# Kernel optimization log

Measured on AMD Instinct MI355X. Metric: run time of the kernel, lower is better.

The kernel has to match this reference:

```python
import jax, jax.numpy as jnp
import numpy as np

B, T = 16, 32768
N_FILTERS, FILTER_LEN = 30, 7


def _stable_coeffs(rng, n_filters, k):
    """Stable IIR denominators (a[0]=1, poles inside unit circle) + random numerators."""
    order = k - 1
    as_list = []
    for _ in range(n_filters):
        radii = rng.uniform(0.5, 0.95, order // 2)
        angles = rng.uniform(0.05, np.pi - 0.05, order // 2)
        poles = radii * np.exp(1j * angles)
        poles = np.concatenate([poles, poles.conj()])
        as_list.append(np.poly(poles).real)  # length k, a[0]=1
    as_ = np.stack(as_list).astype(np.float32)
    bs = (rng.normal(size=(n_filters, k)) * 0.1).astype(np.float32)
    return bs, as_


def setup_inputs() -> dict:
    key = jax.random.key(0)
    x = jax.random.normal(key, (B, T), dtype=jnp.float32)
    rng = np.random.default_rng(0)
    bs, as_ = _stable_coeffs(rng, N_FILTERS, FILTER_LEN)
    return {"x": x, "bs": jnp.asarray(bs), "as_": jnp.asarray(as_)}


def reference(x, bs, as_):
    # x: [B, T]; bs, as_: [F, K]. Output: [B, F, T]
    F, K = bs.shape
    Bb, Tt = x.shape
    a0 = as_[:, :1]
    b = bs / a0
    a_rest = (as_ / a0)[:, 1:]  # [F, K-1]

    # FIR part: fir[b,f,t] = sum_k b[f,k] * x[b, t-k]  (causal convolution)
    lhs = x[:, None, :]                      # [B, 1, T]
    kern = jnp.flip(b, axis=1)[:, None, :]   # [F, 1, K] (flip: conv, not corr)
    fir = jax.lax.conv_general_dilated(
        lhs, kern, window_strides=(1,), padding=[(K - 1, 0)],
        dimension_numbers=("NCH", "OIH", "NCH"))  # [B, F, T]

    # Recursive part: y[t] = fir[t] - sum_{k=1..K-1} a[k] * y[t-k]
    def step(ybuf, fir_t):
        # ybuf: [B, F, K-1] holds y[t-1], ..., y[t-(K-1)]
        y_t = fir_t - jnp.einsum("bfk,fk->bf", ybuf, a_rest)
        ybuf = jnp.concatenate([y_t[:, :, None], ybuf[:, :, :-1]], axis=2)
        return ybuf, y_t

    init = jnp.zeros((Bb, F, K - 1), dtype=x.dtype)
    _, ys = jax.lax.scan(step, init, jnp.moveaxis(fir, 2, 0))  # ys: [T, B, F]
    return jnp.transpose(ys, (1, 2, 0))  # [B, F, T]
```

## Files before the change

kernel.cpp:

```cpp
#include <hip/hip_runtime.h>


#define BB 16
#define TT 32768
#define FF 30
#define KK 7
#define ORD 6
#define CHUNK 64
#define WARM 128
#define CPB 2
#define TSPAN (CPB * CHUNK)
#define NBC (TT / TSPAN)
#define YSTR 132
#define XTILE (WARM + TSPAN)
#define BLK 64

__device__ __forceinline__ float iir_step(float xv, float st[ORD],
                                          const float bcf[KK],
                                          const float acf[ORD]) {
    float y = fmaf(bcf[0], xv, st[0]);
#pragma unroll
    for (int j = 0; j < ORD - 1; ++j)
        st[j] = fmaf(-acf[j], y, fmaf(bcf[j + 1], xv, st[j + 1]));
    st[ORD - 1] = fmaf(-acf[ORD - 1], y, bcf[KK - 1] * xv);
    return y;
}

__global__ __launch_bounds__(BLK) void iir_lds_kernel(
    const float* __restrict__ x,
    const float* __restrict__ bs,
    const float* __restrict__ as_,
    float* __restrict__ out)
{
    __shared__ __align__(16) float ly[FF * YSTR];
    __shared__ __align__(16) float lx[XTILE];

    const int tid = threadIdx.x;
    const int b   = blockIdx.x / NBC;
    const int bc  = blockIdx.x % NBC;
    const int bt0 = bc * TSPAN;
    const int xs  = bt0 - WARM;

    const float* __restrict__ xrow = x + b * TT;

    const int f  = tid % FF;
    const int cl = tid / FF;
    const bool active = tid < FF * CPB;

    float bcf[KK], acf[ORD];
    {
        const int fc = active ? f : 0;
        const float inv_a0 = 1.0f / as_[fc * KK];
#pragma unroll
        for (int j = 0; j < KK; ++j) bcf[j] = bs[fc * KK + j] * inv_a0;
#pragma unroll
        for (int j = 0; j < ORD; ++j) acf[j] = as_[fc * KK + 1 + j] * inv_a0;
    }

    {
        const int t = xs + 4 * tid;
        float4 v = make_float4(0.f, 0.f, 0.f, 0.f);
        if (t >= 0) v = *reinterpret_cast<const float4*>(xrow + t);
        *reinterpret_cast<float4*>(lx + 4 * tid) = v;
    }
    __syncthreads();

    if (active) {
        float st[ORD];
#pragma unroll
        for (int j = 0; j < ORD; ++j) st[j] = 0.0f;

        const float* lxc = lx + cl * CHUNK;

#pragma unroll 8
        for (int s = 0; s < WARM; s += 4) {
            const float4 v = *reinterpret_cast<const float4*>(lxc + s);
            iir_step(v.x, st, bcf, acf);
            iir_step(v.y, st, bcf, acf);
            iir_step(v.z, st, bcf, acf);
            iir_step(v.w, st, bcf, acf);
        }

        float* lyc = ly + f * YSTR + cl * CHUNK;
#pragma unroll 4
        for (int s = 0; s < CHUNK; s += 4) {
            const float4 v = *reinterpret_cast<const float4*>(lxc + WARM + s);
            float4 y;
            y.x = iir_step(v.x, st, bcf, acf);
            y.y = iir_step(v.y, st, bcf, acf);
            y.z = iir_step(v.z, st, bcf, acf);
            y.w = iir_step(v.w, st, bcf, acf);
            *reinterpret_cast<float4*>(lyc + s) = y;
        }
    }
    __syncthreads();

    float* __restrict__ obase = out + b * FF * TT + bt0;
#pragma unroll
    for (int it = 0; it < (FF * TSPAN / 4) / BLK; ++it) {
        const int j  = tid + BLK * it;
        const int fr = j >> 5;
        const int tl = (j & 31) << 2;
        const float4 v = *reinterpret_cast<const float4*>(ly + fr * YSTR + tl);
        *reinterpret_cast<float4*>(obase + fr * TT + tl) = v;
    }
}

extern "C" void kernel_launch(void* const* d_in, const int* in_sizes, int n_in,
                              void* d_out, int out_size, void* d_ws,
                              size_t ws_size, hipStream_t stream) {
    const float* x   = (const float*)d_in[0];
    const float* bs  = (const float*)d_in[1];
    const float* as_ = (const float*)d_in[2];
    float* out = (float*)d_out;

    const int grid = BB * NBC;
    hipLaunchKernelGGL(iir_lds_kernel, dim3(grid), dim3(BLK), 0, stream,
                       x, bs, as_, out);
}
```

Baseline: 29.35 us.

## Interleave two independent IIR chunks per thread and store outputs directly

Each block now covers 256 time steps, and each active thread runs two independent 64-sample chunks (each with a 128-sample warm-up) whose recurrence steps are interleaved to give instruction-level parallelism. The grid is halved. The LDS output staging buffer and the second barrier are removed, so threads write float4 results straight to global memory. In exchange, per-thread global stores are strided across filter rows and coalesce less well, and register pressure rises from the two state vectors.

```diff
diff --git a/kernel.cpp b/kernel.cpp
--- a/kernel.cpp
+++ b/kernel.cpp
@@ -6,13 +6,9 @@
 #define FF 30
 #define KK 7
 #define ORD 6
-#define CHUNK 64
-#define WARM 128
-#define CPB 2
-#define TSPAN (CPB * CHUNK)
+#define TSPAN 256
 #define NBC (TT / TSPAN)
-#define YSTR 132
-#define XTILE (WARM + TSPAN)
+#define XTILE (TSPAN + 128)
 #define BLK 64
 
 __device__ __forceinline__ float iir_step(float xv, float st[ORD],
@@ -26,26 +22,22 @@
     return y;
 }
 
-__global__ __launch_bounds__(BLK) void iir_lds_kernel(
+__global__ __launch_bounds__(BLK, 2) void iir_ilp2_kernel(
     const float* __restrict__ x,
     const float* __restrict__ bs,
     const float* __restrict__ as_,
     float* __restrict__ out)
 {
-    __shared__ __align__(16) float ly[FF * YSTR];
     __shared__ __align__(16) float lx[XTILE];
 
     const int tid = threadIdx.x;
     const int b   = blockIdx.x / NBC;
     const int bc  = blockIdx.x % NBC;
     const int bt0 = bc * TSPAN;
-    const int xs  = bt0 - WARM;
-
-    const float* __restrict__ xrow = x + b * TT;
 
     const int f  = tid % FF;
     const int cl = tid / FF;
-    const bool active = tid < FF * CPB;
+    const bool active = tid < FF * 2;
 
     float bcf[KK], acf[ORD];
     {
@@ -58,51 +50,51 @@
     }
 
     {
-        const int t = xs + 4 * tid;
-        float4 v = make_float4(0.f, 0.f, 0.f, 0.f);
-        if (t >= 0) v = *reinterpret_cast<const float4*>(xrow + t);
-        *reinterpret_cast<float4*>(lx + 4 * tid) = v;
+        const float* __restrict__ xrow = x + b * TT;
+#pragma unroll
+        for (int i = 0; i < 2; ++i) {
+            const int p = i * BLK + tid;
+            if (p < XTILE / 4) {
+                const int t = bt0 - 128 + 4 * p;
+                float4 v = make_float4(0.f, 0.f, 0.f, 0.f);
+                if (t >= 0) v = *reinterpret_cast<const float4*>(xrow + t);
+                *reinterpret_cast<float4*>(lx + 4 * p) = v;
+            }
+        }
     }
     __syncthreads();
 
     if (active) {
-        float st[ORD];
+        const float4* lx4 = reinterpret_cast<const float4*>(lx);
+        const int cA = cl;
+        const int cB = cl + 2;
+
+        float stA[ORD], stB[ORD];
 #pragma unroll
-        for (int j = 0; j < ORD; ++j) st[j] = 0.0f;
+        for (int j = 0; j < ORD; ++j) { stA[j] = 0.0f; stB[j] = 0.0f; }
 
-        const float* lxc = lx + cl * CHUNK;
+        float* __restrict__ orow = out + (b * FF + f) * TT + bt0;
+        float* __restrict__ oA = orow + 64 * cA;
+        float* __restrict__ oB = orow + 64 * cB;
 
-#pragma unroll 8
-        for (int s = 0; s < WARM; s += 4) {
-            const float4 v = *reinterpret_cast<const float4*>(lxc + s);
-            iir_step(v.x, st, bcf, acf);
-            iir_step(v.y, st, bcf, acf);
-            iir_step(v.z, st, bcf, acf);
-            iir_step(v.w, st, bcf, acf);
+#pragma unroll
+        for (int k = 0; k < 48; ++k) {
+            const float4 vA = lx4[16 * cA + k];
+            const float4 vB = lx4[16 * cB + k];
+            float4 yA, yB;
+            yA.x = iir_step(vA.x, stA, bcf, acf);
+            yB.x = iir_step(vB.x, stB, bcf, acf);
+            yA.y = iir_step(vA.y, stA, bcf, acf);
+            yB.y = iir_step(vB.y, stB, bcf, acf);
+            yA.z = iir_step(vA.z, stA, bcf, acf);
+            yB.z = iir_step(vB.z, stB, bcf, acf);
+            yA.w = iir_step(vA.w, stA, bcf, acf);
+            yB.w = iir_step(vB.w, stB, bcf, acf);
+            if (k >= 32) {
+                *reinterpret_cast<float4*>(oA + 4 * (k - 32)) = yA;
+                *reinterpret_cast<float4*>(oB + 4 * (k - 32)) = yB;
+            }
         }
-
-        float* lyc = ly + f * YSTR + cl * CHUNK;
-#pragma unroll 4
-        for (int s = 0; s < CHUNK; s += 4) {
-            const float4 v = *reinterpret_cast<const float4*>(lxc + WARM + s);
-            float4 y;
-            y.x = iir_step(v.x, st, bcf, acf);
-            y.y = iir_step(v.y, st, bcf, acf);
-            y.z = iir_step(v.z, st, bcf, acf);
-            y.w = iir_step(v.w, st, bcf, acf);
-            *reinterpret_cast<float4*>(lyc + s) = y;
-        }
-    }
-    __syncthreads();
-
-    float* __restrict__ obase = out + b * FF * TT + bt0;
-#pragma unroll
-    for (int it = 0; it < (FF * TSPAN / 4) / BLK; ++it) {
-        const int j  = tid + BLK * it;
-        const int fr = j >> 5;
-        const int tl = (j & 31) << 2;
-        const float4 v = *reinterpret_cast<const float4*>(ly + fr * YSTR + tl);
-        *reinterpret_cast<float4*>(obase + fr * TT + tl) = v;
     }
 }
 
@@ -115,6 +107,6 @@
     float* out = (float*)d_out;
 
     const int grid = BB * NBC;
-    hipLaunchKernelGGL(iir_lds_kernel, dim3(grid), dim3(BLK), 0, stream,
+    hipLaunchKernelGGL(iir_ilp2_kernel, dim3(grid), dim3(BLK), 0, stream,
                        x, bs, as_, out);
 }
```

Result: slower. 51.91 us (+76.8%).

## Halve LDS output buffer by staging chunk results in registers and writing per chunk

Applied to the files above, without the earlier changes.

Each thread's filtered output is held in registers (16 float4) instead of written straight to LDS. The chunks then take turns using a half-size LDS tile (YSTR 68) and write it out to global memory. This shrinks shared memory per block, and a launch-bounds hint of 4 is added to raise occupancy. The warmup and output loops are merged into one fully unrolled loop. The cost is more registers per thread and an extra pair of barriers per chunk.

```diff
diff --git a/kernel.cpp b/kernel.cpp
--- a/kernel.cpp
+++ b/kernel.cpp
@@ -7,12 +7,12 @@
 #define KK 7
 #define ORD 6
 #define CHUNK 64
-#define WARM 128
 #define CPB 2
 #define TSPAN (CPB * CHUNK)
 #define NBC (TT / TSPAN)
-#define YSTR 132
+#define WARM 128
 #define XTILE (WARM + TSPAN)
+#define YSTR 68
 #define BLK 64
 
 __device__ __forceinline__ float iir_step(float xv, float st[ORD],
@@ -26,7 +26,7 @@
     return y;
 }
 
-__global__ __launch_bounds__(BLK) void iir_lds_kernel(
+__global__ __launch_bounds__(BLK, 4) void iir_occ_kernel(
     const float* __restrict__ x,
     const float* __restrict__ bs,
     const float* __restrict__ as_,
@@ -39,9 +39,6 @@
     const int b   = blockIdx.x / NBC;
     const int bc  = blockIdx.x % NBC;
     const int bt0 = bc * TSPAN;
-    const int xs  = bt0 - WARM;
-
-    const float* __restrict__ xrow = x + b * TT;
 
     const int f  = tid % FF;
     const int cl = tid / FF;
@@ -58,51 +55,58 @@
     }
 
     {
-        const int t = xs + 4 * tid;
+        const float* __restrict__ xrow = x + b * TT;
+        const int t = bt0 - WARM + 4 * tid;
         float4 v = make_float4(0.f, 0.f, 0.f, 0.f);
         if (t >= 0) v = *reinterpret_cast<const float4*>(xrow + t);
         *reinterpret_cast<float4*>(lx + 4 * tid) = v;
     }
     __syncthreads();
 
+    float4 yreg[16];
     if (active) {
+        const float4* lx4 = reinterpret_cast<const float4*>(lx);
+        const int g0 = 16 * cl;
         float st[ORD];
 #pragma unroll
         for (int j = 0; j < ORD; ++j) st[j] = 0.0f;
 
-        const float* lxc = lx + cl * CHUNK;
-
-#pragma unroll 8
-        for (int s = 0; s < WARM; s += 4) {
-            const float4 v = *reinterpret_cast<const float4*>(lxc + s);
-            iir_step(v.x, st, bcf, acf);
-            iir_step(v.y, st, bcf, acf);
-            iir_step(v.z, st, bcf, acf);
-            iir_step(v.w, st, bcf, acf);
-        }
-
-        float* lyc = ly + f * YSTR + cl * CHUNK;
-#pragma unroll 4
-        for (int s = 0; s < CHUNK; s += 4) {
-            const float4 v = *reinterpret_cast<const float4*>(lxc + WARM + s);
+#pragma unroll
+        for (int k = 0; k < 48; ++k) {
+            const float4 v = lx4[g0 + k];
             float4 y;
             y.x = iir_step(v.x, st, bcf, acf);
             y.y = iir_step(v.y, st, bcf, acf);
             y.z = iir_step(v.z, st, bcf, acf);
             y.w = iir_step(v.w, st, bcf, acf);
-            *reinterpret_cast<float4*>(lyc + s) = y;
+            if (k >= 32) yreg[k - 32] = y;
         }
     }
-    __syncthreads();
 
-    float* __restrict__ obase = out + b * FF * TT + bt0;
+    float* __restrict__ obase0 = out + b * FF * TT + bt0;
 #pragma unroll
-    for (int it = 0; it < (FF * TSPAN / 4) / BLK; ++it) {
-        const int j  = tid + BLK * it;
-        const int fr = j >> 5;
-        const int tl = (j & 31) << 2;
-        const float4 v = *reinterpret_cast<const float4*>(ly + fr * YSTR + tl);
-        *reinterpret_cast<float4*>(obase + fr * TT + tl) = v;
+    for (int p = 0; p < CPB; ++p) {
+        if (active && cl == p) {
+            float* lyc = ly + f * YSTR;
+#pragma unroll
+            for (int k = 0; k < 16; ++k)
+                *reinterpret_cast<float4*>(lyc + 4 * k) = yreg[k];
+        }
+        __syncthreads();
+
+        float* __restrict__ obase = obase0 + p * CHUNK;
+#pragma unroll
+        for (int i = 0; i < 8; ++i) {
+            const int j = i * BLK + tid;
+            if (j < FF * (CHUNK / 4)) {
+                const int fr = j >> 4;
+                const int tl = (j & 15) << 2;
+                const float4 v =
+                    *reinterpret_cast<const float4*>(ly + fr * YSTR + tl);
+                *reinterpret_cast<float4*>(obase + fr * TT + tl) = v;
+            }
+        }
+        __syncthreads();
     }
 }
 
@@ -115,6 +119,6 @@
     float* out = (float*)d_out;
 
     const int grid = BB * NBC;
-    hipLaunchKernelGGL(iir_lds_kernel, dim3(grid), dim3(BLK), 0, stream,
+    hipLaunchKernelGGL(iir_occ_kernel, dim3(grid), dim3(BLK), 0, stream,
                        x, bs, as_, out);
 }
```

Measured after the change: 25.69 us. 12.5% less time.
